# Optimization experiments

Measured on AMD Instinct MI355X. Metric: run time of the kernel, lower is better.

## Reference

```python
import jax, jax.numpy as jnp
import numpy as np

NUM_DAYOFWEEK, NUM_TIME, NUM_MONTH, NUM_DAY = 7, 24, 12, 31
NUM_DESTINATION = 100000
NUM_FACTOR = 128
NUM_DIM = NUM_FACTOR // 4  # 32
N = 1048576


def setup_inputs() -> dict:
    key = jax.random.key(0)
    ks = jax.random.split(key, 10)
    std = 0.1
    return {
        "dayofweek": jax.random.randint(ks[0], (N,), 0, NUM_DAYOFWEEK),
        "time": jax.random.randint(ks[1], (N,), 0, NUM_TIME),
        "month": jax.random.randint(ks[2], (N,), 0, NUM_MONTH),
        "day": jax.random.randint(ks[3], (N,), 0, NUM_DAY),
        "destination": jax.random.randint(ks[4], (N,), 0, NUM_DESTINATION),
        "W_dayofweek": std * jax.random.normal(ks[5], (NUM_DAYOFWEEK, NUM_DIM), dtype=jnp.float32),
        "W_time": std * jax.random.normal(ks[6], (NUM_TIME, NUM_DIM), dtype=jnp.float32),
        "W_month": std * jax.random.normal(ks[7], (NUM_MONTH, NUM_DIM), dtype=jnp.float32),
        "W_day": std * jax.random.normal(ks[8], (NUM_DAY, NUM_DIM), dtype=jnp.float32),
        "W_item": std * jax.random.normal(ks[9], (NUM_DESTINATION, NUM_FACTOR), dtype=jnp.float32),
    }


def reference(dayofweek, time, month, day, destination,
              W_dayofweek, W_time, W_month, W_day, W_item) -> jnp.ndarray:
    # Gather per-feature embeddings and concat into user vector [N, num_factor]
    user = jnp.concatenate([
        W_dayofweek[dayofweek],  # [N, 32]
        W_time[time],            # [N, 32]
        W_month[month],          # [N, 32]
        W_day[day],              # [N, 32]
    ], axis=-1)
    item = W_item[destination]   # [N, 128]
    # Original: diagonal(mm(user, item.T)) == rowwise dot product; compute it directly.
    return jnp.sum(user * item, axis=-1)  # [N]
```

## Files before the change

kernel.cpp:

```cpp
#include <hip/hip_runtime.h>


typedef unsigned long long u64;

constexpr int NDIM = 32;
constexpr int SZ_DOW = 7 * NDIM, SZ_TIM = 24 * NDIM, SZ_MON = 12 * NDIM, SZ_DAY = 31 * NDIM;
constexpr int B_DOW = 0;
constexpr int B_TIM = B_DOW + SZ_DOW;
constexpr int B_MON = B_TIM + SZ_TIM;
constexpr int B_DAY = B_MON + SZ_MON;
constexpr int TAB_TOT = B_DAY + SZ_DAY;

constexpr int NB     = 32;
constexpr int DDIV   = 3125;
constexpr int SLICES = 256;
constexpr int SPB    = 4096;
constexpr int BIN_T  = 1024;
constexpr int IPT    = SPB / BIN_T;
constexpr int CONV_B = 256;

__device__ __forceinline__ unsigned short f2bf(float f) {
    const unsigned u = __float_as_uint(f);
    return (unsigned short)((u + 0x7FFFu + ((u >> 16) & 1u)) >> 16);
}

__device__ __forceinline__ float dot8bf(uint4 a, float4 u0, float4 u1) {
    float s;
    s  = __uint_as_float(a.x << 16)          * u0.x;
    s += __uint_as_float(a.x & 0xFFFF0000u)  * u0.y;
    s += __uint_as_float(a.y << 16)          * u0.z;
    s += __uint_as_float(a.y & 0xFFFF0000u)  * u0.w;
    s += __uint_as_float(a.z << 16)          * u1.x;
    s += __uint_as_float(a.z & 0xFFFF0000u)  * u1.y;
    s += __uint_as_float(a.w << 16)          * u1.z;
    s += __uint_as_float(a.w & 0xFFFF0000u)  * u1.w;
    return s;
}

__device__ __forceinline__ void load_tab(float* tab, const float* Wdow, const float* Wtim,
                                         const float* Wmon, const float* Wday, int nthr) {
    const int t = threadIdx.x;
    for (int i = t; i < SZ_DOW; i += nthr) tab[B_DOW + i] = Wdow[i];
    for (int i = t; i < SZ_TIM; i += nthr) tab[B_TIM + i] = Wtim[i];
    for (int i = t; i < SZ_MON; i += nthr) tab[B_MON + i] = Wmon[i];
    for (int i = t; i < SZ_DAY; i += nthr) tab[B_DAY + i] = Wday[i];
}

__global__ __launch_bounds__(BIN_T)
void prep_kernel(const int* __restrict__ dow, const int* __restrict__ tim,
                 const int* __restrict__ mon, const int* __restrict__ day,
                 const int* __restrict__ dest,
                 int* __restrict__ cntG, int* __restrict__ lbaseG,
                 u64* __restrict__ payload, unsigned short* __restrict__ invl, int n,
                 const float* __restrict__ Witem, unsigned short* __restrict__ Wb,
                 int witem_elems)
{
    const int t = threadIdx.x, b = blockIdx.x;

    if (b >= SLICES) {
        const int nf4 = witem_elems >> 2;
        const float4* src = (const float4*)Witem;
        ushort4* dst = (ushort4*)Wb;
        for (int i = (b - SLICES) * BIN_T + t; i < nf4; i += CONV_B * BIN_T) {
            const float4 v = src[i];
            ushort4 o;
            o.x = f2bf(v.x); o.y = f2bf(v.y); o.z = f2bf(v.z); o.w = f2bf(v.w);
            dst[i] = o;
        }
        return;
    }

    __shared__ u64 stage[SPB];
    __shared__ unsigned short ist[SPB];
    __shared__ int hist[NB], lbase[NB], cursor[NB];

    const int g0 = b * SPB;
    const int rem = n - g0;
    const int len = rem < SPB ? rem : SPB;

    int dreg[IPT], pkreg[IPT];
#pragma unroll
    for (int i = 0; i < IPT; i++) {
        const int k = i * BIN_T + t;
        if (k < len) {
            const int idx = g0 + k;
            dreg[i]  = dest[idx];
            pkreg[i] = dow[idx] | (tim[idx] << 3) | (mon[idx] << 8) | (day[idx] << 12);
        } else { dreg[i] = -1; pkreg[i] = 0; }
    }
    if (t < NB) hist[t] = 0;
    __syncthreads();
#pragma unroll
    for (int i = 0; i < IPT; i++)
        if (dreg[i] >= 0) atomicAdd(&hist[dreg[i] / DDIV], 1);
    __syncthreads();
    if (t == 0) {
        int run = 0;
        for (int q = 0; q < NB; q++) { lbase[q] = run; run += hist[q]; }
    }
    __syncthreads();
    if (t < NB) { cursor[t] = lbase[t]; cntG[b * NB + t] = hist[t]; lbaseG[b * NB + t] = lbase[t]; }
    __syncthreads();
#pragma unroll
    for (int i = 0; i < IPT; i++) {
        const int k = i * BIN_T + t;
        if (k < len) {
            const int j = atomicAdd(&cursor[dreg[i] / DDIV], 1);
            stage[j] = (u64)(unsigned)(g0 + k)
                     | ((u64)(unsigned)dreg[i]  << 20)
                     | ((u64)(unsigned)pkreg[i] << 37);
            ist[k] = (unsigned short)j;
        }
    }
    __syncthreads();
#pragma unroll
    for (int i = 0; i < IPT; i++) {
        const int k = i * BIN_T + t;
        if (k < len) {
            payload[g0 + k] = stage[k];
            invl[g0 + k]    = ist[k];
        }
    }
}

__global__ __launch_bounds__(256, 8)
void mf_main_bf16(const u64* __restrict__ payload,
                  const float* __restrict__ Wdow, const float* __restrict__ Wtim,
                  const float* __restrict__ Wmon, const float* __restrict__ Wday,
                  const unsigned short* __restrict__ Wb,
                  const int* __restrict__ cntG, const int* __restrict__ lbaseG,
                  float* __restrict__ res)
{
    __shared__ float tab[TAB_TOT];
    load_tab(tab, Wdow, Wtim, Wmon, Wday, 256);
    __syncthreads();

    const int tid = threadIdx.x;
    const int sub = tid & 63;
    const int wv  = tid >> 6;
    const int g   = sub >> 3;
    const int l8  = sub & 7;
    const int jt   = l8 >> 1;
    const int half = (l8 & 1) * 16;
    const int tbj  = (jt == 0) ? B_DOW : (jt == 1) ? B_TIM : (jt == 2) ? B_MON : B_DAY;
    const int shj  = (jt == 0) ? 37    : (jt == 1) ? 40    : (jt == 2) ? 45    : 49;
    const int mkj  = (jt == 0) ? 7     : (jt == 1) ? 31    : (jt == 2) ? 15    : 31;

    const int x = blockIdx.x & 7;
    const int s = blockIdx.x >> 3;

    for (int p = 0; p < 4; p++) {
        const int q  = x + 8 * p;
        const int L  = cntG[s * NB + q];
        const int st = s * SPB + lbaseG[s * NB + q];

        for (int i = wv * 16; i < L; i += 64) {
            const int i0 = i + g, i1 = i + 8 + g;
            const bool v0 = i0 < L, v1 = i1 < L;

            const u64 p0 = v0 ? payload[st + i0] : 0ull;
            const u64 p1 = v1 ? payload[st + i1] : 0ull;

            const int d0 = (int)((p0 >> 20) & 0x1FFFFull);
            const int d1 = (int)((p1 >> 20) & 0x1FFFFull);

            const uint4* r0 = (const uint4*)(Wb + (long)d0 * 128 + (l8 << 4));
            const uint4* r1 = (const uint4*)(Wb + (long)d1 * 128 + (l8 << 4));
            const uint4 A0 = r0[0], B0 = r0[1];
            const uint4 A1 = r1[0], B1 = r1[1];

            const int ix0 = (int)((p0 >> shj) & (u64)mkj);
            const int ix1 = (int)((p1 >> shj) & (u64)mkj);
            const float* u0p = &tab[tbj + ix0 * NDIM + half];
            const float* u1p = &tab[tbj + ix1 * NDIM + half];
            const float4 u00 = *(const float4*)(u0p);
            const float4 u01 = *(const float4*)(u0p + 4);
            const float4 u02 = *(const float4*)(u0p + 8);
            const float4 u03 = *(const float4*)(u0p + 12);
            const float4 u10 = *(const float4*)(u1p);
            const float4 u11 = *(const float4*)(u1p + 4);
            const float4 u12 = *(const float4*)(u1p + 8);
            const float4 u13 = *(const float4*)(u1p + 12);

            float a0 = dot8bf(A0, u00, u01) + dot8bf(B0, u02, u03);
            float a1 = dot8bf(A1, u10, u11) + dot8bf(B1, u12, u13);

            a0 += __shfl_xor(a0, 1);  a1 += __shfl_xor(a1, 1);
            a0 += __shfl_xor(a0, 2);  a1 += __shfl_xor(a1, 2);
            a0 += __shfl_xor(a0, 4);  a1 += __shfl_xor(a1, 4);

            if (l8 == 0) {
                if (v0) res[st + i0] = a0;
                if (v1) res[st + i1] = a1;
            }
        }
    }
}

__global__ __launch_bounds__(256, 8)
void mf_main_f32(const u64* __restrict__ payload,
                 const float* __restrict__ Wdow, const float* __restrict__ Wtim,
                 const float* __restrict__ Wmon, const float* __restrict__ Wday,
                 const float* __restrict__ Witem,
                 const int* __restrict__ cntG, const int* __restrict__ lbaseG,
                 float* __restrict__ res)
{
    __shared__ float tab[TAB_TOT];
    load_tab(tab, Wdow, Wtim, Wmon, Wday, 256);
    __syncthreads();

    const int tid = threadIdx.x;
    const int sub = tid & 63;
    const int wv  = tid >> 6;
    const int g   = sub >> 3;
    const int l8  = sub & 7;
    const int col = l8 * 4;
    const int tb[4] = {B_DOW, B_TIM, B_MON, B_DAY};
    const int sh[4] = {37, 40, 45, 49};
    const int mk[4] = {7, 31, 15, 31};

    const int x = blockIdx.x & 7;
    const int s = blockIdx.x >> 3;

    for (int p = 0; p < 4; p++) {
        const int q  = x + 8 * p;
        const int L  = cntG[s * NB + q];
        const int st = s * SPB + lbaseG[s * NB + q];

        for (int i = wv * 16; i < L; i += 64) {
            const int i0 = i + g, i1 = i + 8 + g;
            const bool v0 = i0 < L, v1 = i1 < L;
            const u64 p0 = v0 ? payload[st + i0] : 0ull;
            const u64 p1 = v1 ? payload[st + i1] : 0ull;
            const int d0 = (int)((p0 >> 20) & 0x1FFFFull);
            const int d1 = (int)((p1 >> 20) & 0x1FFFFull);
            const float* r0 = Witem + (long)d0 * 128 + col;
            const float* r1 = Witem + (long)d1 * 128 + col;
            float4 it0[4], it1[4], us0[4], us1[4];
#pragma unroll
            for (int j = 0; j < 4; j++) it0[j] = *reinterpret_cast<const float4*>(r0 + j * NDIM);
#pragma unroll
            for (int j = 0; j < 4; j++) it1[j] = *reinterpret_cast<const float4*>(r1 + j * NDIM);
#pragma unroll
            for (int j = 0; j < 4; j++) {
                const int idx = (int)((p0 >> sh[j]) & (u64)mk[j]);
                us0[j] = *reinterpret_cast<const float4*>(&tab[tb[j] + idx * NDIM + col]);
            }
#pragma unroll
            for (int j = 0; j < 4; j++) {
                const int idx = (int)((p1 >> sh[j]) & (u64)mk[j]);
                us1[j] = *reinterpret_cast<const float4*>(&tab[tb[j] + idx * NDIM + col]);
            }
            float a0 = 0.f, a1 = 0.f;
#pragma unroll
            for (int j = 0; j < 4; j++) {
                a0 += it0[j].x * us0[j].x + it0[j].y * us0[j].y
                    + it0[j].z * us0[j].z + it0[j].w * us0[j].w;
                a1 += it1[j].x * us1[j].x + it1[j].y * us1[j].y
                    + it1[j].z * us1[j].z + it1[j].w * us1[j].w;
            }
            a0 += __shfl_xor(a0, 1);  a1 += __shfl_xor(a1, 1);
            a0 += __shfl_xor(a0, 2);  a1 += __shfl_xor(a1, 2);
            a0 += __shfl_xor(a0, 4);  a1 += __shfl_xor(a1, 4);
            if (l8 == 0) {
                if (v0) res[st + i0] = a0;
                if (v1) res[st + i1] = a1;
            }
        }
    }
}

__global__ __launch_bounds__(BIN_T)
void unperm_kernel(const float* __restrict__ res, const unsigned short* __restrict__ invl,
                   float* __restrict__ out, int n)
{
    __shared__ float r[SPB];
    const int t = threadIdx.x, b = blockIdx.x;
    const int g0 = b * SPB;
    const int rem = n - g0;
    const int len = rem < SPB ? rem : SPB;
    unsigned short iv[IPT];
#pragma unroll
    for (int i = 0; i < IPT; i++) {
        const int k = i * BIN_T + t;
        iv[i] = (k < len) ? invl[g0 + k] : 0;
        if (k < len) r[k] = res[g0 + k];
    }
    __syncthreads();
#pragma unroll
    for (int i = 0; i < IPT; i++) {
        const int k = i * BIN_T + t;
        if (k < len) out[g0 + k] = r[iv[i]];
    }
}

__global__ __launch_bounds__(256, 8)
void mf_dot_kernel(const int* __restrict__ dow, const int* __restrict__ tim,
                   const int* __restrict__ mon, const int* __restrict__ day,
                   const int* __restrict__ dest,
                   const float* __restrict__ Wdow, const float* __restrict__ Wtim,
                   const float* __restrict__ Wmon, const float* __restrict__ Wday,
                   const float* __restrict__ Witem,
                   float* __restrict__ out, int n_samples)
{
    __shared__ float tab[TAB_TOT];
    load_tab(tab, Wdow, Wtim, Wmon, Wday, 256);
    __syncthreads();
    const int tid = threadIdx.x;
    const int lane = tid & 63, sub = lane & 31, wave = tid >> 6, half = lane >> 5;
    const int t = sub >> 3, dofs = (sub & 7) * 4;
    const int* idxp  = (t == 0) ? dow   : (t == 1) ? tim   : (t == 2) ? mon   : day;
    const int  tbase = (t == 0) ? B_DOW : (t == 1) ? B_TIM : (t == 2) ? B_MON : B_DAY;
    long n = (long)blockIdx.x * 8 + wave * 2 + half;
    const long stride = (long)gridDim.x * 8;
    for (; n < n_samples; n += stride) {
        const int idx = idxp[n];
        const int ds  = dest[n];
        const float4 u  = *reinterpret_cast<const float4*>(&tab[tbase + idx * NDIM + dofs]);
        const float4 it = *reinterpret_cast<const float4*>(&Witem[(long)ds * 128 + sub * 4]);
        float r = u.x * it.x + u.y * it.y + u.z * it.z + u.w * it.w;
        r += __shfl_xor(r, 16); r += __shfl_xor(r, 8); r += __shfl_xor(r, 4);
        r += __shfl_xor(r, 2);  r += __shfl_xor(r, 1);
        if (sub == 0) out[n] = r;
    }
}

extern "C" void kernel_launch(void* const* d_in, const int* in_sizes, int n_in,
                              void* d_out, int out_size, void* d_ws, size_t ws_size,
                              hipStream_t stream)
{
    const int*   dow   = (const int*)d_in[0];
    const int*   tim   = (const int*)d_in[1];
    const int*   mon   = (const int*)d_in[2];
    const int*   day   = (const int*)d_in[3];
    const int*   dest  = (const int*)d_in[4];
    const float* Wdow  = (const float*)d_in[5];
    const float* Wtim  = (const float*)d_in[6];
    const float* Wmon  = (const float*)d_in[7];
    const float* Wday  = (const float*)d_in[8];
    const float* Witem = (const float*)d_in[9];
    float* out = (float*)d_out;

    const int n  = in_sizes[0];
    const int we = in_sizes[9];
    const int cap = SLICES * SPB;

    const size_t off_wb       = 64 * 1024;
    const size_t off_pay_full = (off_wb + (size_t)we * 2 + 255) & ~(size_t)255;
    const size_t off_inv_full = off_pay_full + (size_t)cap * 8;
    const size_t off_res_full = off_inv_full + (size_t)cap * 2;
    const size_t need_full    = off_res_full + (size_t)cap * 4;
    const size_t off_pay_mid  = 64 * 1024;
    const size_t off_inv_mid  = off_pay_mid + (size_t)cap * 8;
    const size_t off_res_mid  = off_inv_mid + (size_t)cap * 2;
    const size_t need_mid     = off_res_mid + (size_t)cap * 4;

    if ((size_t)ws_size < need_mid || n > cap) {
        hipLaunchKernelGGL(mf_dot_kernel, dim3(2048), dim3(256), 0, stream,
                           dow, tim, mon, day, dest,
                           Wdow, Wtim, Wmon, Wday, Witem, out, n);
        return;
    }

    const bool full = (size_t)ws_size >= need_full;

    int* cntG   = (int*)d_ws;
    int* lbaseG = (int*)((char*)d_ws + 32 * 1024);
    unsigned short* Wb = full ? (unsigned short*)((char*)d_ws + off_wb) : nullptr;
    u64* payload = (u64*)((char*)d_ws + (full ? off_pay_full : off_pay_mid));
    unsigned short* invl = (unsigned short*)((char*)d_ws + (full ? off_inv_full : off_inv_mid));
    float* res           = (float*)((char*)d_ws + (full ? off_res_full : off_res_mid));

    const int prep_blocks = full ? (SLICES + CONV_B) : SLICES;
    hipLaunchKernelGGL(prep_kernel, dim3(prep_blocks), dim3(BIN_T), 0, stream,
                       dow, tim, mon, day, dest, cntG, lbaseG, payload, invl, n,
                       Witem, Wb, we);
    if (full)
        hipLaunchKernelGGL(mf_main_bf16, dim3(SLICES * 8), dim3(256), 0, stream,
                           payload, Wdow, Wtim, Wmon, Wday, Wb, cntG, lbaseG, res);
    else
        hipLaunchKernelGGL(mf_main_f32, dim3(SLICES * 8), dim3(256), 0, stream,
                           payload, Wdow, Wtim, Wmon, Wday, Witem, cntG, lbaseG, res);
    hipLaunchKernelGGL(unperm_kernel, dim3(SLICES), dim3(BIN_T), 0, stream,
                       res, invl, out, n);
}
```

Before: 153.3 us.

## Fold bf16 conversion into binning blocks, prefetch payload, split unpermute blocks

The W_item fp32-to-bf16 conversion no longer runs in extra dedicated blocks. Each binning block now converts its own slice of the table after loading its indices, so the memory traffic overlaps with the binning latency. The bf16 main loop software-prefetches the next iteration's payload entries, hiding the dependent load before the item gather. The unpermute kernel now uses twice as many blocks, each writing half a slice, to improve parallelism, at the cost of every block reloading the full result slice into shared memory.

After: 156.2 us. About the same (+1.9%).

```diff
diff --git a/kernel.cpp b/kernel.cpp
--- a/kernel.cpp
+++ b/kernel.cpp
@@ -17,7 +17,6 @@
 constexpr int SPB    = 4096;
 constexpr int BIN_T  = 1024;
 constexpr int IPT    = SPB / BIN_T;
-constexpr int CONV_B = 256;
 
 __device__ __forceinline__ unsigned short f2bf(float f) {
     const unsigned u = __float_as_uint(f);
@@ -55,25 +54,11 @@
                  const float* __restrict__ Witem, unsigned short* __restrict__ Wb,
                  int witem_elems)
 {
-    const int t = threadIdx.x, b = blockIdx.x;
-
-    if (b >= SLICES) {
-        const int nf4 = witem_elems >> 2;
-        const float4* src = (const float4*)Witem;
-        ushort4* dst = (ushort4*)Wb;
-        for (int i = (b - SLICES) * BIN_T + t; i < nf4; i += CONV_B * BIN_T) {
-            const float4 v = src[i];
-            ushort4 o;
-            o.x = f2bf(v.x); o.y = f2bf(v.y); o.z = f2bf(v.z); o.w = f2bf(v.w);
-            dst[i] = o;
-        }
-        return;
-    }
-
     __shared__ u64 stage[SPB];
     __shared__ unsigned short ist[SPB];
     __shared__ int hist[NB], lbase[NB], cursor[NB];
 
+    const int t = threadIdx.x, b = blockIdx.x;
     const int g0 = b * SPB;
     const int rem = n - g0;
     const int len = rem < SPB ? rem : SPB;
@@ -88,6 +73,22 @@
             pkreg[i] = dow[idx] | (tim[idx] << 3) | (mon[idx] << 8) | (day[idx] << 12);
         } else { dreg[i] = -1; pkreg[i] = 0; }
     }
+
+    if (Wb) {
+        const int nf4   = witem_elems >> 2;
+        const int chunk = (nf4 + SLICES - 1) / SLICES;
+        const int c0    = b * chunk;
+        const int c1    = min(c0 + chunk, nf4);
+        const float4* src = (const float4*)Witem;
+        ushort4* dst = (ushort4*)Wb;
+        for (int i = c0 + t; i < c1; i += BIN_T) {
+            const float4 v = src[i];
+            ushort4 o;
+            o.x = f2bf(v.x); o.y = f2bf(v.y); o.z = f2bf(v.z); o.w = f2bf(v.w);
+            dst[i] = o;
+        }
+    }
+
     if (t < NB) hist[t] = 0;
     __syncthreads();
 #pragma unroll
@@ -154,23 +155,28 @@
         const int L  = cntG[s * NB + q];
         const int st = s * SPB + lbaseG[s * NB + q];
 
-        for (int i = wv * 16; i < L; i += 64) {
+        int i = wv * 16;
+        u64 p0 = (i + g < L)     ? payload[st + i + g]     : 0ull;
+        u64 p1 = (i + 8 + g < L) ? payload[st + i + 8 + g] : 0ull;
+
+        for (; i < L; i += 64) {
             const int i0 = i + g, i1 = i + 8 + g;
             const bool v0 = i0 < L, v1 = i1 < L;
-
-            const u64 p0 = v0 ? payload[st + i0] : 0ull;
-            const u64 p1 = v1 ? payload[st + i1] : 0ull;
-
-            const int d0 = (int)((p0 >> 20) & 0x1FFFFull);
-            const int d1 = (int)((p1 >> 20) & 0x1FFFFull);
+            const u64 c0 = p0, c1 = p1;
+            const int ni = i + 64;
+            p0 = (ni + g < L)     ? payload[st + ni + g]     : 0ull;
+            p1 = (ni + 8 + g < L) ? payload[st + ni + 8 + g] : 0ull;
+
+            const int d0 = (int)((c0 >> 20) & 0x1FFFFull);
+            const int d1 = (int)((c1 >> 20) & 0x1FFFFull);
 
             const uint4* r0 = (const uint4*)(Wb + (long)d0 * 128 + (l8 << 4));
             const uint4* r1 = (const uint4*)(Wb + (long)d1 * 128 + (l8 << 4));
             const uint4 A0 = r0[0], B0 = r0[1];
             const uint4 A1 = r1[0], B1 = r1[1];
 
-            const int ix0 = (int)((p0 >> shj) & (u64)mkj);
-            const int ix1 = (int)((p1 >> shj) & (u64)mkj);
+            const int ix0 = (int)((c0 >> shj) & (u64)mkj);
+            const int ix1 = (int)((c1 >> shj) & (u64)mkj);
             const float* u0p = &tab[tbj + ix0 * NDIM + half];
             const float* u1p = &tab[tbj + ix1 * NDIM + half];
             const float4 u00 = *(const float4*)(u0p);
@@ -208,7 +214,6 @@
     __shared__ float tab[TAB_TOT];
     load_tab(tab, Wdow, Wtim, Wmon, Wday, 256);
     __syncthreads();
-
     const int tid = threadIdx.x;
     const int sub = tid & 63;
     const int wv  = tid >> 6;
@@ -218,15 +223,12 @@
     const int tb[4] = {B_DOW, B_TIM, B_MON, B_DAY};
     const int sh[4] = {37, 40, 45, 49};
     const int mk[4] = {7, 31, 15, 31};
-
     const int x = blockIdx.x & 7;
     const int s = blockIdx.x >> 3;
-
     for (int p = 0; p < 4; p++) {
         const int q  = x + 8 * p;
         const int L  = cntG[s * NB + q];
         const int st = s * SPB + lbaseG[s * NB + q];
-
         for (int i = wv * 16; i < L; i += 64) {
             const int i0 = i + g, i1 = i + 8 + g;
             const bool v0 = i0 < L, v1 = i1 < L;
@@ -275,21 +277,29 @@
                    float* __restrict__ out, int n)
 {
     __shared__ float r[SPB];
-    const int t = threadIdx.x, b = blockIdx.x;
-    const int g0 = b * SPB;
+    const int t = threadIdx.x;
+    const int w = blockIdx.x >> 1;
+    const int h = blockIdx.x & 1;
+    const int g0 = w * SPB;
     const int rem = n - g0;
     const int len = rem < SPB ? rem : SPB;
-    unsigned short iv[IPT];
+
 #pragma unroll
     for (int i = 0; i < IPT; i++) {
         const int k = i * BIN_T + t;
+        if (k < len) r[k] = res[g0 + k];
+    }
+    const int o0 = h * (SPB / 2);
+    unsigned short iv[IPT / 2];
+#pragma unroll
+    for (int i = 0; i < IPT / 2; i++) {
+        const int k = o0 + i * BIN_T + t;
         iv[i] = (k < len) ? invl[g0 + k] : 0;
-        if (k < len) r[k] = res[g0 + k];
-    }
-    __syncthreads();
-#pragma unroll
-    for (int i = 0; i < IPT; i++) {
-        const int k = i * BIN_T + t;
+    }
+    __syncthreads();
+#pragma unroll
+    for (int i = 0; i < IPT / 2; i++) {
+        const int k = o0 + i * BIN_T + t;
         if (k < len) out[g0 + k] = r[iv[i]];
     }
 }
@@ -371,8 +381,7 @@
     unsigned short* invl = (unsigned short*)((char*)d_ws + (full ? off_inv_full : off_inv_mid));
     float* res           = (float*)((char*)d_ws + (full ? off_res_full : off_res_mid));
 
-    const int prep_blocks = full ? (SLICES + CONV_B) : SLICES;
-    hipLaunchKernelGGL(prep_kernel, dim3(prep_blocks), dim3(BIN_T), 0, stream,
+    hipLaunchKernelGGL(prep_kernel, dim3(SLICES), dim3(BIN_T), 0, stream,
                        dow, tim, mon, day, dest, cntG, lbaseG, payload, invl, n,
                        Witem, Wb, we);
     if (full)
@@ -381,6 +390,6 @@
     else
         hipLaunchKernelGGL(mf_main_f32, dim3(SLICES * 8), dim3(256), 0, stream,
                            payload, Wdow, Wtim, Wmon, Wday, Witem, cntG, lbaseG, res);
-    hipLaunchKernelGGL(unperm_kernel, dim3(SLICES), dim3(BIN_T), 0, stream,
+    hipLaunchKernelGGL(unperm_kernel, dim3(SLICES * 2), dim3(BIN_T), 0, stream,
                        res, invl, out, n);
 }
```
